# Kernel tuning notes

Measured on AMD Instinct MI355X. Metric: run time of the kernel, lower is better.

Reference implementation:

```python
import jax, jax.numpy as jnp
import numpy as np

B, T, H, D_IN = 1048576, 3, 32, 1


def setup_inputs() -> dict:
    key = jax.random.key(0)
    ks = jax.random.split(key, 12)
    s = 1.0 / np.sqrt(H)
    inp = {
        "x": jax.random.normal(ks[0], (B, T, D_IN), dtype=jnp.float32),
        # PyTorch nn.RNN params (weight_ih_l0 [H, D_IN], weight_hh_l0 [H, H])
        "W_ih": jax.random.uniform(ks[1], (H, D_IN), jnp.float32, -s, s),
        "W_hh": jax.random.uniform(ks[2], (H, H), jnp.float32, -s, s),
        "b_ih": jax.random.uniform(ks[3], (H,), jnp.float32, -s, s),
        "b_hh": jax.random.uniform(ks[4], (H,), jnp.float32, -s, s),
        # fc1: Linear(96, 16); fc2: Linear(16, 8); fc3: Linear(8, 1)
        "W1": jax.random.uniform(ks[5], (16, 3 * H), jnp.float32, -1/np.sqrt(3*H), 1/np.sqrt(3*H)),
        "b1": jax.random.uniform(ks[6], (16,), jnp.float32, -1/np.sqrt(3*H), 1/np.sqrt(3*H)),
        "W2": jax.random.uniform(ks[7], (8, 16), jnp.float32, -0.25, 0.25),
        "b2": jax.random.uniform(ks[8], (8,), jnp.float32, -0.25, 0.25),
        "W3": jax.random.uniform(ks[9], (1, 8), jnp.float32, -1/np.sqrt(8), 1/np.sqrt(8)),
        "b3": jax.random.uniform(ks[10], (1,), jnp.float32, -1/np.sqrt(8), 1/np.sqrt(8)),
    }
    return inp


def reference(x, W_ih, W_hh, b_ih, b_hh, W1, b1, W2, b2, W3, b3):
    # Vanilla RNN: h_t = tanh(x_t W_ih^T + b_ih + h_{t-1} W_hh^T + b_hh), h_0 = 0
    def step(h, xt):
        h = jnp.tanh(xt @ W_ih.T + b_ih + h @ W_hh.T + b_hh)
        return h, h

    h0 = jnp.zeros((x.shape[0], W_hh.shape[0]), dtype=x.dtype)
    _, hs = jax.lax.scan(step, h0, jnp.swapaxes(x, 0, 1))  # hs: [T, B, H]
    out = jax.nn.relu(jnp.swapaxes(hs, 0, 1))              # [B, T, H]
    out = out.reshape(out.shape[0], -1)                    # [B, T*H] = [B, 96]
    out = out @ W1.T + b1                                  # fc1 -> 16
    out = jax.nn.relu(out @ W2.T + b2)                     # fc2 -> 8, relu
    return out @ W3.T + b3                                 # fc3 -> 1
```

## Files before the change

### kernel.cpp

```cpp
#include <hip/hip_runtime.h>

typedef _Float16 f16x8 __attribute__((ext_vector_type(8)));
typedef __fp16  fp16x2 __attribute__((ext_vector_type(2)));
typedef float f32x16 __attribute__((ext_vector_type(16)));

union FU { unsigned u[4]; f16x8 v; };

__device__ __forceinline__ unsigned pkrtz(float a, float b) {
    union { fp16x2 h; unsigned u; } c;
    c.h = __builtin_amdgcn_cvt_pkrtz(a, b);
    return c.u;
}
__device__ __forceinline__ float f16bits_to_f32(unsigned u16bits) {
    union { unsigned short s; _Float16 h; } c; c.s = (unsigned short)u16bits;
    return (float)c.h;
}
__device__ __forceinline__ unsigned pk_rtn(float a, float b) {
    union { _Float16 h[2]; unsigned u; } c;
    c.h[0] = (_Float16)a; c.h[1] = (_Float16)b;
    return c.u;
}

__device__ __forceinline__ float tanh_fast(float ap) {
    float e = __builtin_amdgcn_exp2f(ap);
    return fmaf(-2.0f, __builtin_amdgcn_rcpf(e + 1.0f), 1.0f);
}

__global__ __launch_bounds__(256, 2)
void rnn_mlp_kernel(const float* __restrict__ x,
                    const float* __restrict__ wih, const float* __restrict__ whh,
                    const float* __restrict__ bih, const float* __restrict__ bhh,
                    const float* __restrict__ w1,  const float* __restrict__ b1,
                    const float* __restrict__ w2,  const float* __restrict__ b2,
                    const float* __restrict__ w3,  const float* __restrict__ b3,
                    float* __restrict__ out, int B)
{
    const float K = 2.8853900817779268f;
    const int tid = threadIdx.x;
    const int wv = tid >> 6, l = tid & 63;
    const int n = l & 31, H = l >> 5;

    f32x16 zeroC;
    #pragma unroll
    for (int r = 0; r < 16; ++r) zeroC[r] = 0.f;

    FU xcA;
    {
        const unsigned w0 = pkrtz(wih[n] * K, (bih[n] + bhh[n]) * K);
        xcA.u[0] = (H == 0) ? w0 : 0u;
        xcA.u[1] = 0u; xcA.u[2] = 0u; xcA.u[3] = 0u;
    }
    FU whhF[2][2];
    #pragma unroll
    for (int c = 0; c < 2; ++c)
        #pragma unroll
        for (int r = 0; r < 4; ++r) {
            const int j0 = c * 16 + 4 * H + 8 * (r >> 1) + 2 * (r & 1);
            const float a0 = whh[n * 32 + j0]     * K;
            const float a1 = whh[n * 32 + j0 + 1] * K;
            const unsigned hi = pkrtz(a0, a1);
            whhF[c][0].u[r] = hi;
            whhF[c][1].u[r] = pkrtz(a0 - f16bits_to_f32(hi & 0xffffu),
                                    a1 - f16bits_to_f32(hi >> 16));
        }
    FU w1F[3][2];
    #pragma unroll
    for (int tt = 0; tt < 3; ++tt)
        #pragma unroll
        for (int c = 0; c < 2; ++c)
            #pragma unroll
            for (int r = 0; r < 4; ++r) {
                const int j0 = c * 16 + 4 * H + 8 * (r >> 1) + 2 * (r & 1);
                const float a0 = (n < 16) ? w1[n * 96 + tt * 32 + j0]     : 0.f;
                const float a1 = (n < 16) ? w1[n * 96 + tt * 32 + j0 + 1] : 0.f;
                w1F[tt][c].u[r] = pkrtz(a0, a1);
            }
    FU w2F;
    #pragma unroll
    for (int r = 0; r < 4; ++r) {
        const int k0 = 4 * H + 8 * (r >> 1) + 2 * (r & 1);
        const float a0 = (n < 8) ? w2[n * 16 + k0]     : 0.f;
        const float a1 = (n < 8) ? w2[n * 16 + k0 + 1] : 0.f;
        w2F.u[r] = pkrtz(a0, a1);
    }
    float b2p[4], w3v[4];
    #pragma unroll
    for (int r = 0; r < 4; ++r) {
        const int o = r + 4 * H;
        float s = b2[o];
        #pragma unroll
        for (int k = 0; k < 16; ++k) s = fmaf(w2[o * 16 + k], b1[k], s);
        b2p[r] = s;
        w3v[r] = w3[o];
    }
    const float b3s = b3[0];

    const int WSTRIDE = gridDim.x * 4 * 64;
    int base0 = (blockIdx.x * 4 + wv) * 64;

    float nx[2][3];
    #pragma unroll
    for (int z = 0; z < 2; ++z) {
        const int v = base0 + 32 * z + n;
        const int ix = (v < B) ? v : (B - 1);
        nx[z][0] = x[3*ix]; nx[z][1] = x[3*ix+1]; nx[z][2] = x[3*ix+2];
    }

    for (; base0 < B; base0 += WSTRIDE) {
        float xv[2][3];
        #pragma unroll
        for (int z = 0; z < 2; ++z) {
            xv[z][0] = nx[z][0]; xv[z][1] = nx[z][1]; xv[z][2] = nx[z][2];
        }

        const int nb = base0 + WSTRIDE;
        if (nb < B) {
            #pragma unroll
            for (int z = 0; z < 2; ++z) {
                const int v = nb + 32 * z + n;
                const int ix = (v < B) ? v : (B - 1);
                nx[z][0] = x[3*ix]; nx[z][1] = x[3*ix+1]; nx[z][2] = x[3*ix+2];
            }
        }

        f32x16 f1a[2], f1b[2];
        FU hF[2][2];

        #pragma unroll
        for (int t = 0; t < 3; ++t) {
            f32x16 av[2];
            #pragma unroll
            for (int z = 0; z < 2; ++z) {
                FU xcB;
                const unsigned w0 = pk_rtn(xv[z][t], 1.0f);
                xcB.u[0] = (H == 0) ? w0 : 0u;
                xcB.u[1] = 0u; xcB.u[2] = 0u; xcB.u[3] = 0u;
                av[z] = __builtin_amdgcn_mfma_f32_32x32x16_f16(xcA.v, xcB.v, zeroC, 0,0,0);
            }
            if (t > 0) {
                #pragma unroll
                for (int z = 0; z < 2; ++z) {
                    av[z] = __builtin_amdgcn_mfma_f32_32x32x16_f16(whhF[0][0].v, hF[z][0].v, av[z], 0,0,0);
                    av[z] = __builtin_amdgcn_mfma_f32_32x32x16_f16(whhF[0][1].v, hF[z][0].v, av[z], 0,0,0);
                    av[z] = __builtin_amdgcn_mfma_f32_32x32x16_f16(whhF[1][0].v, hF[z][1].v, av[z], 0,0,0);
                    av[z] = __builtin_amdgcn_mfma_f32_32x32x16_f16(whhF[1][1].v, hF[z][1].v, av[z], 0,0,0);
                }
            }

            FU rF[2][2];
            #pragma unroll
            for (int z = 0; z < 2; ++z) {
                float h[16];
                #pragma unroll
                for (int r = 0; r < 16; ++r) h[r] = tanh_fast(av[z][r]);
                #pragma unroll
                for (int c = 0; c < 2; ++c)
                    #pragma unroll
                    for (int w = 0; w < 4; ++w) {
                        const float v0 = h[2*w + 8*c], v1 = h[2*w + 8*c + 1];
                        if (t < 2) hF[z][c].u[w] = pkrtz(v0, v1);
                        rF[z][c].u[w] = pkrtz(fmaxf(v0, 0.f), fmaxf(v1, 0.f));
                    }
            }

            #pragma unroll
            for (int z = 0; z < 2; ++z) {
                if (t == 0) {
                    f1a[z] = __builtin_amdgcn_mfma_f32_32x32x16_f16(w1F[t][0].v, rF[z][0].v, zeroC, 0,0,0);
                    f1b[z] = __builtin_amdgcn_mfma_f32_32x32x16_f16(w1F[t][1].v, rF[z][1].v, zeroC, 0,0,0);
                } else {
                    f1a[z] = __builtin_amdgcn_mfma_f32_32x32x16_f16(w1F[t][0].v, rF[z][0].v, f1a[z], 0,0,0);
                    f1b[z] = __builtin_amdgcn_mfma_f32_32x32x16_f16(w1F[t][1].v, rF[z][1].v, f1b[z], 0,0,0);
                }
            }
        }

        #pragma unroll
        for (int z = 0; z < 2; ++z) {
            FU bB;
            #pragma unroll
            for (int w = 0; w < 4; ++w)
                bB.u[w] = pkrtz(f1a[z][2*w] + f1b[z][2*w], f1a[z][2*w+1] + f1b[z][2*w+1]);
            f32x16 gacc = __builtin_amdgcn_mfma_f32_32x32x16_f16(w2F.v, bB.v, zeroC, 0,0,0);

            float p = 0.f;
            #pragma unroll
            for (int r = 0; r < 4; ++r)
                p = fmaf(fmaxf(gacc[r] + b2p[r], 0.f), w3v[r], p);
            const float y = p + __shfl_xor(p, 32) + b3s;
            const int idx = base0 + 32 * z + n;
            if (H == 0 && idx < B) out[idx] = y;
        }
    }
}

extern "C" void kernel_launch(void* const* d_in, const int* in_sizes, int n_in,
                              void* d_out, int out_size, void* d_ws, size_t ws_size,
                              hipStream_t stream)
{
    const float* x   = (const float*)d_in[0];
    const float* wih = (const float*)d_in[1];
    const float* whh = (const float*)d_in[2];
    const float* bih = (const float*)d_in[3];
    const float* bhh = (const float*)d_in[4];
    const float* w1  = (const float*)d_in[5];
    const float* b1  = (const float*)d_in[6];
    const float* w2  = (const float*)d_in[7];
    const float* b2  = (const float*)d_in[8];
    const float* w3  = (const float*)d_in[9];
    const float* b3  = (const float*)d_in[10];
    float* out = (float*)d_out;

    const int B = in_sizes[0] / 3;

    int blocks = (B + 255) / 256;
    if (blocks > 1024) blocks = 1024;
    rnn_mlp_kernel<<<blocks, 256, 0, stream>>>(x, wih, whh, bih, bhh,
                                               w1, b1, w2, b2, w3, b3, out, B);
}
```

Before: 113.1 us.

## Drop split-fp16 recurrent weights, use single fp16 W_hh and packed ReLU

Removes the hi/lo fp16 split of the recurrent weight matrix, cutting recurrent MFMAs per step from four to two per sub-tile. Weights are now rounded to nearest instead of toward zero. ReLU is applied as a packed fp16 max on the already-converted hidden state instead of separate float max and conversion. The two fc1 accumulators are merged into one chain, removing the final add. This lowers precision of the recurrence and serializes the fc1 MFMA chain, which may raise error against the reference.

```diff
diff --git a/kernel.cpp b/kernel.cpp
--- a/kernel.cpp
+++ b/kernel.cpp
@@ -10,10 +10,6 @@
     union { fp16x2 h; unsigned u; } c;
     c.h = __builtin_amdgcn_cvt_pkrtz(a, b);
     return c.u;
-}
-__device__ __forceinline__ float f16bits_to_f32(unsigned u16bits) {
-    union { unsigned short s; _Float16 h; } c; c.s = (unsigned short)u16bits;
-    return (float)c.h;
 }
 __device__ __forceinline__ unsigned pk_rtn(float a, float b) {
     union { _Float16 h[2]; unsigned u; } c;
@@ -43,6 +39,7 @@
     f32x16 zeroC;
     #pragma unroll
     for (int r = 0; r < 16; ++r) zeroC[r] = 0.f;
+    const f16x8 zf = {0, 0, 0, 0, 0, 0, 0, 0};
 
     FU xcA;
     {
@@ -50,18 +47,13 @@
         xcA.u[0] = (H == 0) ? w0 : 0u;
         xcA.u[1] = 0u; xcA.u[2] = 0u; xcA.u[3] = 0u;
     }
-    FU whhF[2][2];
+    FU whhF[2];
     #pragma unroll
     for (int c = 0; c < 2; ++c)
         #pragma unroll
         for (int r = 0; r < 4; ++r) {
             const int j0 = c * 16 + 4 * H + 8 * (r >> 1) + 2 * (r & 1);
-            const float a0 = whh[n * 32 + j0]     * K;
-            const float a1 = whh[n * 32 + j0 + 1] * K;
-            const unsigned hi = pkrtz(a0, a1);
-            whhF[c][0].u[r] = hi;
-            whhF[c][1].u[r] = pkrtz(a0 - f16bits_to_f32(hi & 0xffffu),
-                                    a1 - f16bits_to_f32(hi >> 16));
+            whhF[c].u[r] = pk_rtn(whh[n * 32 + j0] * K, whh[n * 32 + j0 + 1] * K);
         }
     FU w1F[3][2];
     #pragma unroll
@@ -73,7 +65,7 @@
                 const int j0 = c * 16 + 4 * H + 8 * (r >> 1) + 2 * (r & 1);
                 const float a0 = (n < 16) ? w1[n * 96 + tt * 32 + j0]     : 0.f;
                 const float a1 = (n < 16) ? w1[n * 96 + tt * 32 + j0 + 1] : 0.f;
-                w1F[tt][c].u[r] = pkrtz(a0, a1);
+                w1F[tt][c].u[r] = pk_rtn(a0, a1);
             }
     FU w2F;
     #pragma unroll
@@ -81,7 +73,7 @@
         const int k0 = 4 * H + 8 * (r >> 1) + 2 * (r & 1);
         const float a0 = (n < 8) ? w2[n * 16 + k0]     : 0.f;
         const float a1 = (n < 8) ? w2[n * 16 + k0 + 1] : 0.f;
-        w2F.u[r] = pkrtz(a0, a1);
+        w2F.u[r] = pk_rtn(a0, a1);
     }
     float b2p[4], w3v[4];
     #pragma unroll
@@ -123,7 +115,7 @@
             }
         }
 
-        f32x16 f1a[2], f1b[2];
+        f32x16 f1[2];
         FU hF[2][2];
 
         #pragma unroll
@@ -140,10 +132,8 @@
             if (t > 0) {
                 #pragma unroll
                 for (int z = 0; z < 2; ++z) {
-                    av[z] = __builtin_amdgcn_mfma_f32_32x32x16_f16(whhF[0][0].v, hF[z][0].v, av[z], 0,0,0);
-                    av[z] = __builtin_amdgcn_mfma_f32_32x32x16_f16(whhF[0][1].v, hF[z][0].v, av[z], 0,0,0);
-                    av[z] = __builtin_amdgcn_mfma_f32_32x32x16_f16(whhF[1][0].v, hF[z][1].v, av[z], 0,0,0);
-                    av[z] = __builtin_amdgcn_mfma_f32_32x32x16_f16(whhF[1][1].v, hF[z][1].v, av[z], 0,0,0);
+                    av[z] = __builtin_amdgcn_mfma_f32_32x32x16_f16(whhF[0].v, hF[z][0].v, av[z], 0,0,0);
+                    av[z] = __builtin_amdgcn_mfma_f32_32x32x16_f16(whhF[1].v, hF[z][1].v, av[z], 0,0,0);
                 }
             }
 
@@ -154,24 +144,21 @@
                 #pragma unroll
                 for (int r = 0; r < 16; ++r) h[r] = tanh_fast(av[z][r]);
                 #pragma unroll
-                for (int c = 0; c < 2; ++c)
+                for (int c = 0; c < 2; ++c) {
+                    FU tF;
                     #pragma unroll
-                    for (int w = 0; w < 4; ++w) {
-                        const float v0 = h[2*w + 8*c], v1 = h[2*w + 8*c + 1];
-                        if (t < 2) hF[z][c].u[w] = pkrtz(v0, v1);
-                        rF[z][c].u[w] = pkrtz(fmaxf(v0, 0.f), fmaxf(v1, 0.f));
-                    }
-            }
-
-            #pragma unroll
-            for (int z = 0; z < 2; ++z) {
-                if (t == 0) {
-                    f1a[z] = __builtin_amdgcn_mfma_f32_32x32x16_f16(w1F[t][0].v, rF[z][0].v, zeroC, 0,0,0);
-                    f1b[z] = __builtin_amdgcn_mfma_f32_32x32x16_f16(w1F[t][1].v, rF[z][1].v, zeroC, 0,0,0);
-                } else {
-                    f1a[z] = __builtin_amdgcn_mfma_f32_32x32x16_f16(w1F[t][0].v, rF[z][0].v, f1a[z], 0,0,0);
-                    f1b[z] = __builtin_amdgcn_mfma_f32_32x32x16_f16(w1F[t][1].v, rF[z][1].v, f1b[z], 0,0,0);
+                    for (int w = 0; w < 4; ++w)
+                        tF.u[w] = pkrtz(h[2*w + 8*c], h[2*w + 8*c + 1]);
+                    if (t < 2) hF[z][c] = tF;
+                    rF[z][c].v = __builtin_elementwise_max(tF.v, zf);
                 }
+            }
+
+            #pragma unroll
+            for (int z = 0; z < 2; ++z) {
+                f1[z] = __builtin_amdgcn_mfma_f32_32x32x16_f16(w1F[t][0].v, rF[z][0].v,
+                                                               (t == 0) ? zeroC : f1[z], 0,0,0);
+                f1[z] = __builtin_amdgcn_mfma_f32_32x32x16_f16(w1F[t][1].v, rF[z][1].v, f1[z], 0,0,0);
             }
         }
 
@@ -180,7 +167,7 @@
             FU bB;
             #pragma unroll
             for (int w = 0; w < 4; ++w)
-                bB.u[w] = pkrtz(f1a[z][2*w] + f1b[z][2*w], f1a[z][2*w+1] + f1b[z][2*w+1]);
+                bB.u[w] = pkrtz(f1[z][2*w], f1[z][2*w+1]);
             f32x16 gacc = __builtin_amdgcn_mfma_f32_32x32x16_f16(w2F.v, bB.v, zeroC, 0,0,0);
 
             float p = 0.f;
```

After: 118.1 us. 1.04x slower.
